# Kernel tuning notes

Hardware: AMD Instinct MI355X
Metric: run time of the kernel (lower is better)

Reference implementation:

```python
import jax, jax.numpy as jnp
import numpy as np

B, T_E, T_D, H = 32, 128, 128, 256  # batch, encoder len, decoder len, hidden


def lstm_scan(x, h0, c0, Wih, Whh, bih, bhh):
    """Single-layer PyTorch-style LSTM over x: [B, T, F] -> (hs, cs) each [T, B, H]."""
    bias = bih + bhh

    def step(carry, xt):
        h, c = carry
        gates = xt @ Wih.T + h @ Whh.T + bias  # [B, 4H], gate order i,f,g,o
        i, f, g, o = jnp.split(gates, 4, axis=-1)
        i = jax.nn.sigmoid(i)
        f = jax.nn.sigmoid(f)
        o = jax.nn.sigmoid(o)
        g = jnp.tanh(g)
        c = f * c + i * g
        h = o * jnp.tanh(c)
        return (h, c), (h, c)

    _, (hs, cs) = jax.lax.scan(step, (h0, c0), jnp.swapaxes(x, 0, 1))
    return hs, cs


def setup_inputs() -> dict:
    key = jax.random.key(0)
    ks = jax.random.split(key, 16)
    seq = jax.random.normal(ks[0], (B, T_E), jnp.float32)
    seq_m = jax.random.randint(ks[1], (B, 1), 1, T_E + 1)  # valid lengths in [1, T_E]
    pos = jnp.arange(T_E)[None, :]
    seq = jnp.where(pos < seq_m, seq, 0.0)  # zero-pad beyond length (drives the mask)
    target = jax.random.normal(ks[2], (B, T_D), jnp.float32)

    s = 0.1
    nrm = lambda k, shape: s * jax.random.normal(k, shape, jnp.float32)
    return dict(
        seq=seq, seq_m=seq_m, target=target,
        Wih_e=nrm(ks[3], (4 * H, 1)), Whh_e=nrm(ks[4], (4 * H, H)),
        bih_e=nrm(ks[5], (4 * H,)), bhh_e=nrm(ks[6], (4 * H,)),
        Wih_d=nrm(ks[7], (4 * H, 1)), Whh_d=nrm(ks[8], (4 * H, H)),
        bih_d=nrm(ks[9], (4 * H,)), bhh_d=nrm(ks[10], (4 * H,)),
        We=nrm(ks[11], (H, H)), be=nrm(ks[12], (H,)),
        Wd=nrm(ks[13], (H, H)), bd=nrm(ks[14], (H,)),
        v=jnp.ones((H,), jnp.float32),
    )


def reference(seq, seq_m, target,
              Wih_e, Whh_e, bih_e, bhh_e,
              Wih_d, Whh_d, bih_d, bhh_d,
              We, be, Wd, bd, v):
    zeros = jnp.zeros((B, H), seq.dtype)
    # Encoder: one fused scan instead of the original per-timestep Python loop
    hs_e, cs_e = lstm_scan(seq[..., None], zeros, zeros, Wih_e, Whh_e, bih_e, bhh_e)
    e = jnp.swapaxes(hs_e, 0, 1)  # [B, T_E, H]

    # Grab encoder state at the last valid step (seq_m - 1) per batch element
    last = seq_m[:, 0] - 1  # [B]
    bidx = jnp.arange(B)
    e_hs = hs_e[last, bidx]  # [B, H]
    e_cs = cs_e[last, bidx]

    # Decoder initialized from the selected encoder state
    hs_d, _ = lstm_scan(target[..., None], e_hs, e_cs, Wih_d, Whh_d, bih_d, bhh_d)
    d = jnp.swapaxes(hs_d, 0, 1)  # [B, T_D, H]

    e2 = e @ We.T + be  # [B, T_E, H]
    d2 = d @ Wd.T + bd  # [B, T_D, H]

    # Additive (Bahdanau) attention: tanh(e_j + d_i) . v  -> [B, T_D, T_E]
    t = jnp.tanh(d2[:, :, None, :] + e2[:, None, :, :])  # [B, T_D, T_E, H]
    p = jnp.einsum('bijh,h->bij', t, v)

    # Masking: original sets seq[:,0]=0.1 then adds 1000 where seq value nonzero,
    # after subtracting 1000 everywhere -> padded (zero) positions end up at -1000.
    seq0 = seq.at[:, 0].set(0.1)
    mask = (seq0 != 0).astype(p.dtype)  # [B, T_E]
    p = p + (mask[:, None, :] - 1.0) * 1000.0

    return jax.nn.softmax(p, axis=-1)  # pointer distribution over encoder positions
```

## Files before the change

kernel.cpp:

```cpp
#include <hip/hip_runtime.h>
#include <hip/hip_bf16.h>

#define BB 32
#define TT 128
#define HH 256
#define G4 4
#define UPB 64
#define RPB 256

#define AGENT __HIP_MEMORY_SCOPE_AGENT
#define AL(p) __hip_atomic_load((p), __ATOMIC_RELAXED, AGENT)

__device__ __forceinline__ float rcp_f(float x) { return __builtin_amdgcn_rcpf(x); }
__device__ __forceinline__ float sigmoid_f(float x) {
    return rcp_f(1.f + __expf(-x));
}
__device__ __forceinline__ float tanh_f(float x) {
    float e = __expf(2.f * x);
    return 1.f - 2.f * rcp_f(e + 1.f);
}

__global__ __launch_bounds__(512, 2) void lstm_kernel(
    const float* __restrict__ seq,
    const int* __restrict__ seq_m,
    const float* __restrict__ target,
    const float* __restrict__ Wih_e,
    const float* __restrict__ Whh_e,
    const float* __restrict__ bih_e, const float* __restrict__ bhh_e,
    const float* __restrict__ Wih_d, const float* __restrict__ Whh_d,
    const float* __restrict__ bih_d, const float* __restrict__ bhh_d,
    const float* __restrict__ We, const float* __restrict__ be,
    const float* __restrict__ Wd, const float* __restrict__ bd,
    float* __restrict__ e2,
    float* __restrict__ d2,
    unsigned long long* __restrict__ mbox,
    unsigned long long* __restrict__ hsave)
{
    const int blk = blockIdx.x;
    const int b = blk & 31;
    const int g = blk >> 5;
    const int tid = threadIdx.x;
    const int row_local = tid >> 1;
    const int half = tid & 1;
    const int gate = row_local >> 6;
    const int u_local = row_local & 63;
    const int row_global = gate * HH + g * UPB + u_local;
    const int last = seq_m[b] - 1;
    const int s = tid - 256;
    const int pu = s >> 2;
    const int kq = s & 3;
    const int pcol = g * UPB + pu;

    __shared__ float hbuf[2][HH];
    __shared__ float g_lds[RPB];
    __shared__ float x_lds[2 * TT];
    __shared__ float h_final[HH];

    for (int i = tid; i < TT; i += 512) {
        x_lds[i] = seq[b * TT + i];
        x_lds[TT + i] = target[b * TT + i];
    }

    float4 w[32];
    float bias_r, wih_r;
    auto loadw = [&](const float* Whh, const float* Wih,
                     const float* bih, const float* bhh) {
        const float4* wr = (const float4*)(Whh + row_global * HH + half * 128);
#pragma unroll
        for (int i = 0; i < 32; ++i) w[i] = wr[i];
        bias_r = bih[row_global] + bhh[row_global];
        wih_r = Wih[row_global];
    };
    loadw(Whh_e, Wih_e, bih_e, bhh_e);

    float4 pw[16];
    float pb = 0.f;
    auto loadp = [&](const float* W, const float* bias) {
        const float4* src = (const float4*)(W + pcol * HH + kq * 64);
#pragma unroll
        for (int i = 0; i < 16; ++i) pw[i] = src[i];
        pb = bias[pcol];
    };
    if (tid >= 256) loadp(We, be);

    if (tid < 64) {
        ((float4*)hbuf[1])[tid] = make_float4(0.f, 0.f, 0.f, 0.f);
    }
    __syncthreads();

    float c = 0.f, c_saved = 0.f, h_saved = 0.f;

    for (int t = 0; t < 2 * TT; ++t) {
        const int phase = t >> 7;
        const int tt = t & 127;
        const float x = x_lds[t];
        const int rb = (t & 1) ^ 1;

        const float4* h4 = ((const float4*)hbuf[rb]) + half * 32;
        float4 a4 = make_float4(0.f, 0.f, 0.f, 0.f);
#pragma unroll
        for (int i = 0; i < 32; ++i) {
            float4 hv = h4[i];
            a4.x = fmaf(w[i].x, hv.x, a4.x);
            a4.y = fmaf(w[i].y, hv.y, a4.y);
            a4.z = fmaf(w[i].z, hv.z, a4.z);
            a4.w = fmaf(w[i].w, hv.w, a4.w);
        }
        float acc = (a4.x + a4.y) + (a4.z + a4.w);
        acc += __shfl_xor(acc, 1);
        float gv = acc + bias_r + x * wih_r;
        if (half == 0) g_lds[row_local] = gv;
        __syncthreads();

        if (tid < 64) {
            float gi = g_lds[tid];
            float gf = g_lds[64 + tid];
            float gg = g_lds[128 + tid];
            float go = g_lds[192 + tid];
            float si = sigmoid_f(gi);
            float sf = sigmoid_f(gf);
            float tg = tanh_f(gg);
            float so = sigmoid_f(go);
            c = sf * c + si * tg;
            float h = so * tanh_f(c);
            const int ug = g * UPB + tid;
            unsigned long long pkt =
                ((unsigned long long)(unsigned)(t + 1) << 32) | __float_as_uint(h);
            __hip_atomic_store(&mbox[(t & 1) * BB * HH + b * HH + ug], pkt,
                               __ATOMIC_RELAXED, AGENT);
            if (phase == 0 && tt == last) {
                c_saved = c;
                h_saved = h;
                unsigned long long spkt =
                    (1ull << 32) | (unsigned long long)__float_as_uint(h);
                __hip_atomic_store(&hsave[b * HH + ug], spkt, __ATOMIC_RELAXED, AGENT);
            }
            hbuf[t & 1][ug] = (t == TT - 1) ? h_saved : h;
        }

        if (tid >= 64 && tid < 256) {
            const int p = (g + (tid >> 6)) & 3;
            const int lane = tid & 63;
            const int ppu = p * UPB + lane;
            unsigned long long* src;
            unsigned want;
            if (t == TT - 1) {
                src = &hsave[b * HH + ppu];
                want = 1u;
            } else {
                src = &mbox[(t & 1) * BB * HH + b * HH + ppu];
                want = (unsigned)(t + 1);
            }
            unsigned long long pv;
            {
                unsigned long long r0 = AL(src);
                unsigned long long r1 = AL(src);
                unsigned long long r2 = AL(src);
                unsigned long long r3 = AL(src);
                for (;;) {
                    if ((unsigned)(r0 >> 32) == want) { pv = r0; break; }
                    r0 = AL(src);
                    if ((unsigned)(r1 >> 32) == want) { pv = r1; break; }
                    r1 = AL(src);
                    if ((unsigned)(r2 >> 32) == want) { pv = r2; break; }
                    r2 = AL(src);
                    if ((unsigned)(r3 >> 32) == want) { pv = r3; break; }
                    r3 = AL(src);
                }
            }
            hbuf[t & 1][ppu] = __uint_as_float((unsigned)pv);
        }

        if (tid >= 256 && t >= 1) {
            const float* hsrc = (t == TT) ? h_final : hbuf[rb];
            const float4* hp = (const float4*)(hsrc + kq * 64);
            float pa = 0.f;
#pragma unroll
            for (int i = 0; i < 16; ++i) {
                float4 hv = hp[i];
                pa = fmaf(pw[i].x, hv.x, pa);
                pa = fmaf(pw[i].y, hv.y, pa);
                pa = fmaf(pw[i].z, hv.z, pa);
                pa = fmaf(pw[i].w, hv.w, pa);
            }
            pa += __shfl_xor(pa, 1);
            pa += __shfl_xor(pa, 2);
            if (kq == 0) {
                if (t <= TT)
                    e2[(b * TT + (t - 1)) * HH + pcol] = pa + pb;
                else
                    d2[(b * TT + (t - 1 - TT)) * HH + pcol] = pa + pb;
            }
        }
        if (tid >= 256 && t == TT - 1) {
            unsigned long long* src = &mbox[((TT - 1) & 1) * BB * HH + b * HH + s];
            const unsigned want = (unsigned)TT;
            unsigned long long r0 = AL(src);
            unsigned long long r1 = AL(src);
            unsigned long long pv;
            for (;;) {
                if ((unsigned)(r0 >> 32) == want) { pv = r0; break; }
                r0 = AL(src);
                if ((unsigned)(r1 >> 32) == want) { pv = r1; break; }
                r1 = AL(src);
            }
            h_final[s] = __uint_as_float((unsigned)pv);
        }
        if (tid >= 256 && t == TT) loadp(Wd, bd);

        __syncthreads();

        if (t == TT - 1) {
            loadw(Whh_d, Wih_d, bih_d, bhh_d);
            c = c_saved;
        }
    }

    if (tid >= 256) {
        unsigned long long* src = &mbox[((2 * TT - 1) & 1) * BB * HH + b * HH + s];
        const unsigned want = (unsigned)(2 * TT);
        unsigned long long r0 = AL(src);
        unsigned long long r1 = AL(src);
        unsigned long long pv;
        for (;;) {
            if ((unsigned)(r0 >> 32) == want) { pv = r0; break; }
            r0 = AL(src);
            if ((unsigned)(r1 >> 32) == want) { pv = r1; break; }
            r1 = AL(src);
        }
        h_final[s] = __uint_as_float((unsigned)pv);
    }
    __syncthreads();
    if (tid >= 256) {
        const float4* hp = (const float4*)(h_final + kq * 64);
        float pa = 0.f;
#pragma unroll
        for (int i = 0; i < 16; ++i) {
            float4 hv = hp[i];
            pa = fmaf(pw[i].x, hv.x, pa);
            pa = fmaf(pw[i].y, hv.y, pa);
            pa = fmaf(pw[i].z, hv.z, pa);
            pa = fmaf(pw[i].w, hv.w, pa);
        }
        pa += __shfl_xor(pa, 1);
        pa += __shfl_xor(pa, 2);
        if (kq == 0) d2[(b * TT + (TT - 1)) * HH + pcol] = pa + pb;
    }
}

#define EPAD 260
#define PPAD 132
__global__ __launch_bounds__(256) void attn_kernel(
    const float* __restrict__ e2, const float* __restrict__ d2,
    const float* __restrict__ vv, const float* __restrict__ seq,
    float* __restrict__ out) {
    __shared__ float e2c[32][EPAD];
    __shared__ float d2t[32][EPAD];
    __shared__ float p_lds[32][PPAD];
    __shared__ float v_lds[HH];

    const int blk = blockIdx.x;
    const int b = blk >> 2;
    const int i0 = (blk & 3) * 32;
    const int tid = threadIdx.x;
    const int jl = tid & 31, ig = tid >> 5;

    if (tid < 64) *(float4*)&v_lds[tid * 4] = ((const float4*)vv)[tid];
    for (int idx = tid; idx < 32 * 64; idx += 256) {
        int r = idx >> 6, q = idx & 63;
        *(float4*)&d2t[r][q * 4] = ((const float4*)(d2 + (b * TT + i0 + r) * HH))[q];
    }

    for (int jc = 0; jc < TT; jc += 32) {
        __syncthreads();
        for (int idx = tid; idx < 32 * 64; idx += 256) {
            int r = idx >> 6, q = idx & 63;
            *(float4*)&e2c[r][q * 4] = ((const float4*)(e2 + (b * TT + jc + r) * HH))[q];
        }
        __syncthreads();

        float a0 = 0.f, a1 = 0.f, a2 = 0.f, a3 = 0.f;
        for (int h = 0; h < HH; h += 4) {
            float4 ev = *(const float4*)&e2c[jl][h];
            float4 vx = *(const float4*)&v_lds[h];
            float4 d0 = *(const float4*)&d2t[ig * 4 + 0][h];
            float4 d1 = *(const float4*)&d2t[ig * 4 + 1][h];
            float4 d2v = *(const float4*)&d2t[ig * 4 + 2][h];
            float4 d3 = *(const float4*)&d2t[ig * 4 + 3][h];
            a0 = fmaf(tanh_f(ev.x + d0.x), vx.x, a0);
            a0 = fmaf(tanh_f(ev.y + d0.y), vx.y, a0);
            a0 = fmaf(tanh_f(ev.z + d0.z), vx.z, a0);
            a0 = fmaf(tanh_f(ev.w + d0.w), vx.w, a0);
            a1 = fmaf(tanh_f(ev.x + d1.x), vx.x, a1);
            a1 = fmaf(tanh_f(ev.y + d1.y), vx.y, a1);
            a1 = fmaf(tanh_f(ev.z + d1.z), vx.z, a1);
            a1 = fmaf(tanh_f(ev.w + d1.w), vx.w, a1);
            a2 = fmaf(tanh_f(ev.x + d2v.x), vx.x, a2);
            a2 = fmaf(tanh_f(ev.y + d2v.y), vx.y, a2);
            a2 = fmaf(tanh_f(ev.z + d2v.z), vx.z, a2);
            a2 = fmaf(tanh_f(ev.w + d2v.w), vx.w, a2);
            a3 = fmaf(tanh_f(ev.x + d3.x), vx.x, a3);
            a3 = fmaf(tanh_f(ev.y + d3.y), vx.y, a3);
            a3 = fmaf(tanh_f(ev.z + d3.z), vx.z, a3);
            a3 = fmaf(tanh_f(ev.w + d3.w), vx.w, a3);
        }
        const int j = jc + jl;
        float sv = (j == 0) ? 0.1f : seq[b * TT + j];
        float msk = (sv == 0.f) ? -1000.f : 0.f;
        p_lds[ig * 4 + 0][j] = a0 + msk;
        p_lds[ig * 4 + 1][j] = a1 + msk;
        p_lds[ig * 4 + 2][j] = a2 + msk;
        p_lds[ig * 4 + 3][j] = a3 + msk;
    }
    __syncthreads();

    const int r = tid >> 3, l8 = tid & 7;
    float xr[16];
    float m = -1e30f;
#pragma unroll
    for (int k = 0; k < 16; ++k) {
        xr[k] = p_lds[r][l8 + 8 * k];
        m = fmaxf(m, xr[k]);
    }
#pragma unroll
    for (int o = 4; o >= 1; o >>= 1) m = fmaxf(m, __shfl_xor(m, o));
    float s = 0.f;
#pragma unroll
    for (int k = 0; k < 16; ++k) {
        xr[k] = __expf(xr[k] - m);
        s += xr[k];
    }
#pragma unroll
    for (int o = 4; o >= 1; o >>= 1) s += __shfl_xor(s, o);
    float inv = rcp_f(s);
    float* orow = out + (b * TT + i0 + r) * TT;
#pragma unroll
    for (int k = 0; k < 16; ++k) orow[l8 + 8 * k] = xr[k] * inv;
}

extern "C" void kernel_launch(void* const* d_in, const int* in_sizes, int n_in,
                              void* d_out, int out_size, void* d_ws, size_t ws_size,
                              hipStream_t stream) {
    const float* seq = (const float*)d_in[0];
    const int* seq_m = (const int*)d_in[1];
    const float* target = (const float*)d_in[2];
    const float* Wih_e = (const float*)d_in[3];
    const float* Whh_e = (const float*)d_in[4];
    const float* bih_e = (const float*)d_in[5];
    const float* bhh_e = (const float*)d_in[6];
    const float* Wih_d = (const float*)d_in[7];
    const float* Whh_d = (const float*)d_in[8];
    const float* bih_d = (const float*)d_in[9];
    const float* bhh_d = (const float*)d_in[10];
    const float* We = (const float*)d_in[11];
    const float* be = (const float*)d_in[12];
    const float* Wd = (const float*)d_in[13];
    const float* bd = (const float*)d_in[14];
    const float* vv = (const float*)d_in[15];

    float* ws = (float*)d_ws;
    const size_t SZ_ED = (size_t)BB * TT * HH;
    float* e2 = ws;
    float* d2 = e2 + SZ_ED;
    unsigned long long* mbox = (unsigned long long*)(d2 + SZ_ED);
    unsigned long long* hsave = mbox + 2 * BB * HH;

    const size_t needed =
        2 * SZ_ED * sizeof(float) + 3 * BB * HH * sizeof(unsigned long long);
    if (ws_size < needed) return;

    hipMemsetAsync(mbox, 0, 3 * BB * HH * sizeof(unsigned long long), stream);
    lstm_kernel<<<BB * G4, 512, 0, stream>>>(seq, seq_m, target, Wih_e, Whh_e, bih_e,
                                             bhh_e, Wih_d, Whh_d, bih_d, bhh_d, We,
                                             be, Wd, bd, e2, d2, mbox, hsave);
    attn_kernel<<<BB * 4, 256, 0, stream>>>(e2, d2, vv, seq, (float*)d_out);
}
```

Measured before the change: 647.2 us.

## Split attention into score and softmax kernels and stagger projection reads

The attention stage is split in two. A scores kernel runs on 512 blocks, each handling one 32x32 tile of (decoder, encoder) positions, and writes the raw scores to a workspace buffer. A separate softmax kernel then applies the mask and normalises each row. This gives about four times more blocks than the old 128-block fused kernel, which should fill the GPU's compute units better, at the cost of one extra launch and a global round trip for the scores. The projection dot product in the LSTM kernel now uses a loop rotated by lane group, to stagger shared-memory reads and reduce bank conflicts.

Measured after the change: 1.495 ms. 2.31x slower.

```diff
diff --git a/kernel.cpp b/kernel.cpp
--- a/kernel.cpp
+++ b/kernel.cpp
@@ -83,6 +83,23 @@
     };
     if (tid >= 256) loadp(We, be);
 
+    auto projdot = [&](const float* hsrc) -> float {
+        const float4* hp = (const float4*)(hsrc + kq * 64);
+        float pa = 0.f;
+#pragma unroll
+        for (int i = 0; i < 16; ++i) {
+            const int idx = (i + 2 * kq) & 15;
+            float4 hv = hp[idx];
+            pa = fmaf(pw[idx].x, hv.x, pa);
+            pa = fmaf(pw[idx].y, hv.y, pa);
+            pa = fmaf(pw[idx].z, hv.z, pa);
+            pa = fmaf(pw[idx].w, hv.w, pa);
+        }
+        pa += __shfl_xor(pa, 1);
+        pa += __shfl_xor(pa, 2);
+        return pa + pb;
+    };
+
     if (tid < 64) {
         ((float4*)hbuf[1])[tid] = make_float4(0.f, 0.f, 0.f, 0.f);
     }
@@ -173,23 +190,12 @@
 
         if (tid >= 256 && t >= 1) {
             const float* hsrc = (t == TT) ? h_final : hbuf[rb];
-            const float4* hp = (const float4*)(hsrc + kq * 64);
-            float pa = 0.f;
-#pragma unroll
-            for (int i = 0; i < 16; ++i) {
-                float4 hv = hp[i];
-                pa = fmaf(pw[i].x, hv.x, pa);
-                pa = fmaf(pw[i].y, hv.y, pa);
-                pa = fmaf(pw[i].z, hv.z, pa);
-                pa = fmaf(pw[i].w, hv.w, pa);
-            }
-            pa += __shfl_xor(pa, 1);
-            pa += __shfl_xor(pa, 2);
+            float pv = projdot(hsrc);
             if (kq == 0) {
                 if (t <= TT)
-                    e2[(b * TT + (t - 1)) * HH + pcol] = pa + pb;
+                    e2[(b * TT + (t - 1)) * HH + pcol] = pv;
                 else
-                    d2[(b * TT + (t - 1 - TT)) * HH + pcol] = pa + pb;
+                    d2[(b * TT + (t - 1 - TT)) * HH + pcol] = pv;
             }
         }
         if (tid >= 256 && t == TT - 1) {
@@ -232,36 +238,23 @@
     }
     __syncthreads();
     if (tid >= 256) {
-        const float4* hp = (const float4*)(h_final + kq * 64);
-        float pa = 0.f;
-#pragma unroll
-        for (int i = 0; i < 16; ++i) {
-            float4 hv = hp[i];
-            pa = fmaf(pw[i].x, hv.x, pa);
-            pa = fmaf(pw[i].y, hv.y, pa);
-            pa = fmaf(pw[i].z, hv.z, pa);
-            pa = fmaf(pw[i].w, hv.w, pa);
-        }
-        pa += __shfl_xor(pa, 1);
-        pa += __shfl_xor(pa, 2);
-        if (kq == 0) d2[(b * TT + (TT - 1)) * HH + pcol] = pa + pb;
+        float pv = projdot(h_final);
+        if (kq == 0) d2[(b * TT + (TT - 1)) * HH + pcol] = pv;
     }
 }
 
 #define EPAD 260
-#define PPAD 132
-__global__ __launch_bounds__(256) void attn_kernel(
+__global__ __launch_bounds__(256) void attn_p_kernel(
     const float* __restrict__ e2, const float* __restrict__ d2,
-    const float* __restrict__ vv, const float* __restrict__ seq,
-    float* __restrict__ out) {
+    const float* __restrict__ vv, float* __restrict__ p_ws) {
     __shared__ float e2c[32][EPAD];
     __shared__ float d2t[32][EPAD];
-    __shared__ float p_lds[32][PPAD];
     __shared__ float v_lds[HH];
 
     const int blk = blockIdx.x;
-    const int b = blk >> 2;
-    const int i0 = (blk & 3) * 32;
+    const int b = blk >> 4;
+    const int i0 = ((blk >> 2) & 3) * 32;
+    const int j0 = (blk & 3) * 32;
     const int tid = threadIdx.x;
     const int jl = tid & 31, ig = tid >> 5;
 
@@ -269,73 +262,76 @@
     for (int idx = tid; idx < 32 * 64; idx += 256) {
         int r = idx >> 6, q = idx & 63;
         *(float4*)&d2t[r][q * 4] = ((const float4*)(d2 + (b * TT + i0 + r) * HH))[q];
-    }
-
-    for (int jc = 0; jc < TT; jc += 32) {
-        __syncthreads();
-        for (int idx = tid; idx < 32 * 64; idx += 256) {
-            int r = idx >> 6, q = idx & 63;
-            *(float4*)&e2c[r][q * 4] = ((const float4*)(e2 + (b * TT + jc + r) * HH))[q];
-        }
-        __syncthreads();
-
-        float a0 = 0.f, a1 = 0.f, a2 = 0.f, a3 = 0.f;
-        for (int h = 0; h < HH; h += 4) {
-            float4 ev = *(const float4*)&e2c[jl][h];
-            float4 vx = *(const float4*)&v_lds[h];
-            float4 d0 = *(const float4*)&d2t[ig * 4 + 0][h];
-            float4 d1 = *(const float4*)&d2t[ig * 4 + 1][h];
-            float4 d2v = *(const float4*)&d2t[ig * 4 + 2][h];
-            float4 d3 = *(const float4*)&d2t[ig * 4 + 3][h];
-            a0 = fmaf(tanh_f(ev.x + d0.x), vx.x, a0);
-            a0 = fmaf(tanh_f(ev.y + d0.y), vx.y, a0);
-            a0 = fmaf(tanh_f(ev.z + d0.z), vx.z, a0);
-            a0 = fmaf(tanh_f(ev.w + d0.w), vx.w, a0);
-            a1 = fmaf(tanh_f(ev.x + d1.x), vx.x, a1);
-            a1 = fmaf(tanh_f(ev.y + d1.y), vx.y, a1);
-            a1 = fmaf(tanh_f(ev.z + d1.z), vx.z, a1);
-            a1 = fmaf(tanh_f(ev.w + d1.w), vx.w, a1);
-            a2 = fmaf(tanh_f(ev.x + d2v.x), vx.x, a2);
-            a2 = fmaf(tanh_f(ev.y + d2v.y), vx.y, a2);
-            a2 = fmaf(tanh_f(ev.z + d2v.z), vx.z, a2);
-            a2 = fmaf(tanh_f(ev.w + d2v.w), vx.w, a2);
-            a3 = fmaf(tanh_f(ev.x + d3.x), vx.x, a3);
-            a3 = fmaf(tanh_f(ev.y + d3.y), vx.y, a3);
-            a3 = fmaf(tanh_f(ev.z + d3.z), vx.z, a3);
-            a3 = fmaf(tanh_f(ev.w + d3.w), vx.w, a3);
-        }
-        const int j = jc + jl;
+        *(float4*)&e2c[r][q * 4] = ((const float4*)(e2 + (b * TT + j0 + r) * HH))[q];
+    }
+    __syncthreads();
+
+    float a0 = 0.f, a1 = 0.f, a2 = 0.f, a3 = 0.f;
+    for (int h = 0; h < HH; h += 4) {
+        float4 ev = *(const float4*)&e2c[jl][h];
+        float4 vx = *(const float4*)&v_lds[h];
+        float4 d0 = *(const float4*)&d2t[ig * 4 + 0][h];
+        float4 d1 = *(const float4*)&d2t[ig * 4 + 1][h];
+        float4 d2v = *(const float4*)&d2t[ig * 4 + 2][h];
+        float4 d3 = *(const float4*)&d2t[ig * 4 + 3][h];
+        a0 = fmaf(tanh_f(ev.x + d0.x), vx.x, a0);
+        a0 = fmaf(tanh_f(ev.y + d0.y), vx.y, a0);
+        a0 = fmaf(tanh_f(ev.z + d0.z), vx.z, a0);
+        a0 = fmaf(tanh_f(ev.w + d0.w), vx.w, a0);
+        a1 = fmaf(tanh_f(ev.x + d1.x), vx.x, a1);
+        a1 = fmaf(tanh_f(ev.y + d1.y), vx.y, a1);
+        a1 = fmaf(tanh_f(ev.z + d1.z), vx.z, a1);
+        a1 = fmaf(tanh_f(ev.w + d1.w), vx.w, a1);
+        a2 = fmaf(tanh_f(ev.x + d2v.x), vx.x, a2);
+        a2 = fmaf(tanh_f(ev.y + d2v.y), vx.y, a2);
+        a2 = fmaf(tanh_f(ev.z + d2v.z), vx.z, a2);
+        a2 = fmaf(tanh_f(ev.w + d2v.w), vx.w, a2);
+        a3 = fmaf(tanh_f(ev.x + d3.x), vx.x, a3);
+        a3 = fmaf(tanh_f(ev.y + d3.y), vx.y, a3);
+        a3 = fmaf(tanh_f(ev.z + d3.z), vx.z, a3);
+        a3 = fmaf(tanh_f(ev.w + d3.w), vx.w, a3);
+    }
+    float* pr = p_ws + (b * TT + i0 + ig * 4) * TT + j0 + jl;
+    pr[0 * TT] = a0;
+    pr[1 * TT] = a1;
+    pr[2 * TT] = a2;
+    pr[3 * TT] = a3;
+}
+
+__global__ __launch_bounds__(256) void attn_sm_kernel(
+    const float* __restrict__ p_ws, const float* __restrict__ seq,
+    float* __restrict__ out) {
+    const int blk = blockIdx.x;
+    const int b = blk >> 3;
+    const int r0 = (blk & 7) * 16;
+    const int tid = threadIdx.x;
+    const int r = tid >> 4, l16 = tid & 15;
+    const int row = (b * TT + r0 + r) * TT;
+
+    float xr[8];
+    float m = -1e30f;
+#pragma unroll
+    for (int k = 0; k < 8; ++k) {
+        const int j = l16 + 16 * k;
+        float x = p_ws[row + j];
         float sv = (j == 0) ? 0.1f : seq[b * TT + j];
-        float msk = (sv == 0.f) ? -1000.f : 0.f;
-        p_lds[ig * 4 + 0][j] = a0 + msk;
-        p_lds[ig * 4 + 1][j] = a1 + msk;
-        p_lds[ig * 4 + 2][j] = a2 + msk;
-        p_lds[ig * 4 + 3][j] = a3 + msk;
-    }
-    __syncthreads();
-
-    const int r = tid >> 3, l8 = tid & 7;
-    float xr[16];
-    float m = -1e30f;
-#pragma unroll
-    for (int k = 0; k < 16; ++k) {
-        xr[k] = p_lds[r][l8 + 8 * k];
-        m = fmaxf(m, xr[k]);
-    }
-#pragma unroll
-    for (int o = 4; o >= 1; o >>= 1) m = fmaxf(m, __shfl_xor(m, o));
+        if (sv == 0.f) x -= 1000.f;
+        xr[k] = x;
+        m = fmaxf(m, x);
+    }
+#pragma unroll
+    for (int o = 8; o >= 1; o >>= 1) m = fmaxf(m, __shfl_xor(m, o));
     float s = 0.f;
 #pragma unroll
-    for (int k = 0; k < 16; ++k) {
+    for (int k = 0; k < 8; ++k) {
         xr[k] = __expf(xr[k] - m);
         s += xr[k];
     }
 #pragma unroll
-    for (int o = 4; o >= 1; o >>= 1) s += __shfl_xor(s, o);
+    for (int o = 8; o >= 1; o >>= 1) s += __shfl_xor(s, o);
     float inv = rcp_f(s);
-    float* orow = out + (b * TT + i0 + r) * TT;
-#pragma unroll
-    for (int k = 0; k < 16; ++k) orow[l8 + 8 * k] = xr[k] * inv;
+#pragma unroll
+    for (int k = 0; k < 8; ++k) out[row + l16 + 16 * k] = xr[k] * inv;
 }
 
 extern "C" void kernel_launch(void* const* d_in, const int* in_sizes, int n_in,
@@ -362,16 +358,19 @@
     const size_t SZ_ED = (size_t)BB * TT * HH;
     float* e2 = ws;
     float* d2 = e2 + SZ_ED;
-    unsigned long long* mbox = (unsigned long long*)(d2 + SZ_ED);
+    float* p_ws = d2 + SZ_ED;
+    unsigned long long* mbox =
+        (unsigned long long*)(p_ws + (size_t)BB * TT * TT);
     unsigned long long* hsave = mbox + 2 * BB * HH;
 
-    const size_t needed =
-        2 * SZ_ED * sizeof(float) + 3 * BB * HH * sizeof(unsigned long long);
+    const size_t needed = (2 * SZ_ED + (size_t)BB * TT * TT) * sizeof(float) +
+                          3 * BB * HH * sizeof(unsigned long long);
     if (ws_size < needed) return;
 
     hipMemsetAsync(mbox, 0, 3 * BB * HH * sizeof(unsigned long long), stream);
     lstm_kernel<<<BB * G4, 512, 0, stream>>>(seq, seq_m, target, Wih_e, Whh_e, bih_e,
                                              bhh_e, Wih_d, Whh_d, bih_d, bhh_d, We,
                                              be, Wd, bd, e2, d2, mbox, hsave);
-    attn_kernel<<<BB * 4, 256, 0, stream>>>(e2, d2, vv, seq, (float*)d_out);
-}
+    attn_p_kernel<<<512, 256, 0, stream>>>(e2, d2, vv, p_ws);
+    attn_sm_kernel<<<256, 256, 0, stream>>>(p_ws, seq, (float*)d_out);
+}
```
